# Kernel tuning notes

Hardware: AMD Instinct MI355X
Metric: run time of the kernel (lower is better)

## Reference

```python
import jax, jax.numpy as jnp
import numpy as np


def setup_inputs() -> dict:
    key = jax.random.key(0)
    k1, k2 = jax.random.split(key)
    B, K, S = 262144, 32, 30
    sparse_code = jax.random.normal(k1, (B, K), dtype=jnp.float32)
    dictionary = jax.random.normal(k2, (S * S, K), dtype=jnp.float32)
    return {"sparse_code": sparse_code, "dictionary": dictionary, "image_size": S}


def reference(sparse_code, dictionary, image_size):
    # matmul(dictionary, sparse_code.T).T == sparse_code @ dictionary.T -> [B, S*S]
    samples = jnp.einsum("bk,dk->bd", sparse_code, dictionary)
    B = samples.shape[0]
    img = samples.reshape(B, image_size, image_size)
    # Serpentine unrolling: flip every odd row (rows 1,3,...,image_size-1)
    img = img.at[:, 1::2, :].set(img[:, 1::2, ::-1])
    return img[:, None, :, :]  # [B, 1, S, S]
```

## Files before the change

kernel.cpp:

```cpp
#include <hip/hip_runtime.h>
#include <hip/hip_bf16.h>


typedef __attribute__((ext_vector_type(8))) short bf16x8;
typedef __attribute__((ext_vector_type(4))) float f32x4;

constexpr int KD    = 32;
constexpr int DDIM  = 900;
constexpr int SDIM  = 30;
constexpr int NCHT  = 57;
constexpr int TROWS = 16;
constexpr int TILES = 16;
constexpr int RPB   = TROWS * TILES;
constexpr int TFL   = TROWS * DDIM;

__device__ __forceinline__ int serp_src(int d) {
    int r = d / SDIM, c = d - r * SDIM;
    return (r & 1) ? (r * SDIM + (SDIM - 1 - c)) : d;
}

__device__ __forceinline__ short f2bf(float x) {
    __hip_bfloat16 h = __float2bfloat16(x);
    short u; __builtin_memcpy(&u, &h, 2); return u;
}

__device__ __forceinline__ void barrier_lds() {
    __builtin_amdgcn_sched_barrier(0);
    asm volatile("s_waitcnt lgkmcnt(0)" ::: "memory");
    __builtin_amdgcn_sched_barrier(0);
    __builtin_amdgcn_s_barrier();
    __builtin_amdgcn_sched_barrier(0);
}

__global__ __launch_bounds__(256, 1) void mfma_decode(
    const float* __restrict__ sc,
    const float* __restrict__ dict,
    float* __restrict__ out,
    int B)
{
    __shared__ alignas(16) float stg[2][TFL];

    const int t    = threadIdx.x;
    const int lane = t & 63;
    const int wid  = t >> 6;

    const int brow = lane & 15;
    const int k0   = (lane >> 4) << 3;
    const int dloc = (lane >> 4) << 2;
    const long long b0 = (long long)blockIdx.x * RPB;

    float4 ra[TILES], rb[TILES];
    #pragma unroll
    for (int tt = 0; tt < TILES; ++tt) {
        const float* ap = sc + (size_t)(b0 + tt * TROWS + brow) * KD + k0;
        ra[tt] = *reinterpret_cast<const float4*>(ap);
        rb[tt] = *reinterpret_cast<const float4*>(ap + 4);
    }

    bf16x8 df[15];
    #pragma unroll
    for (int j = 0; j < 15; ++j) {
        int ch = wid + 4 * j; if (ch > NCHT - 1) ch = NCHT - 1;
        int d  = ch * 16 + (lane & 15);
        int dd = (d < DDIM) ? d : (DDIM - 1);
        const float* p = dict + (size_t)serp_src(dd) * KD + k0;
        const float4 f0 = *reinterpret_cast<const float4*>(p);
        const float4 f1 = *reinterpret_cast<const float4*>(p + 4);
        bf16x8 a;
        a[0] = f2bf(f0.x); a[1] = f2bf(f0.y); a[2] = f2bf(f0.z); a[3] = f2bf(f0.w);
        a[4] = f2bf(f1.x); a[5] = f2bf(f1.y); a[6] = f2bf(f1.z); a[7] = f2bf(f1.w);
        df[j] = a;
    }

    bf16x8 bb[TILES];
    #pragma unroll
    for (int tt = 0; tt < TILES; ++tt) {
        bf16x8 r;
        r[0] = f2bf(ra[tt].x); r[1] = f2bf(ra[tt].y);
        r[2] = f2bf(ra[tt].z); r[3] = f2bf(ra[tt].w);
        r[4] = f2bf(rb[tt].x); r[5] = f2bf(rb[tt].y);
        r[6] = f2bf(rb[tt].z); r[7] = f2bf(rb[tt].w);
        bb[tt] = r;
    }

    auto compute = [&](const bf16x8& bbx, float* buf) {
        #pragma unroll
        for (int j = 0; j < 15; ++j) {
            const int ch = wid + 4 * j;
            if (ch < NCHT) {
                f32x4 z = {0.f, 0.f, 0.f, 0.f};
                f32x4 acc = __builtin_amdgcn_mfma_f32_16x16x32_bf16(df[j], bbx, z, 0, 0, 0);
                if (ch != 56) {
                    *reinterpret_cast<f32x4*>(&buf[brow * DDIM + ch * 16 + dloc]) = acc;
                } else if (dloc == 0) {
                    *reinterpret_cast<f32x4*>(&buf[brow * DDIM + 896]) = acc;
                }
            }
        }
    };

    compute(bb[0], stg[0]);
    barrier_lds();

    const int base = t * 4;

    #pragma unroll
    for (int tile = 0; tile < TILES; ++tile) {
        if (tile + 1 < TILES) compute(bb[tile + 1], stg[(tile + 1) & 1]);

        float* __restrict__ tbase = out + (size_t)(b0 + (long long)tile * TROWS) * DDIM;
        const float* __restrict__ buf = stg[tile & 1];
        #pragma unroll
        for (int i = 0; i < 14; ++i) {
            const int o = i * 1024 + base;
            f32x4 v = *reinterpret_cast<const f32x4*>(&buf[o]);
            *reinterpret_cast<f32x4*>(tbase + o) = v;
        }
        if (t < 16) {
            const int o = 14336 + base;
            f32x4 v = *reinterpret_cast<const f32x4*>(&buf[o]);
            *reinterpret_cast<f32x4*>(tbase + o) = v;
        }

        if (tile + 1 < TILES) barrier_lds();
    }
}

extern "C" void kernel_launch(void* const* d_in, const int* in_sizes, int n_in,
                              void* d_out, int out_size, void* d_ws, size_t ws_size,
                              hipStream_t stream) {
    const float* sc   = (const float*)d_in[0];
    const float* dict = (const float*)d_in[1];
    float* out        = (float*)d_out;

    const int B = in_sizes[0] / KD;

    mfma_decode<<<dim3((unsigned)(B / RPB)), 256, 0, stream>>>(sc, dict, out, B);
}
```

Baseline: 194.9 us.

## Specialize warps into MFMA producers and global-store consumers with 512 threads

The block doubles to 512 threads. Waves 0-3 load the dictionary and codes, run the MFMA tiles and write them into double-buffered LDS, while waves 4-7 only copy finished tiles from LDS to global memory. The aim is to overlap compute with the store-bound output traffic through producer/consumer specialization. The cost is an extra barrier per tile, and the store loop now has half the waves doing all the writes, which may reduce store parallelism per wave.

After: 195.1 us. About the same (+0.1%).

```diff
diff --git a/kernel.cpp b/kernel.cpp
--- a/kernel.cpp
+++ b/kernel.cpp
@@ -32,7 +32,7 @@
     __builtin_amdgcn_sched_barrier(0);
 }
 
-__global__ __launch_bounds__(256, 1) void mfma_decode(
+__global__ __launch_bounds__(512, 1) void mfma_decode(
     const float* __restrict__ sc,
     const float* __restrict__ dict,
     float* __restrict__ out,
@@ -49,39 +49,8 @@
     const int dloc = (lane >> 4) << 2;
     const long long b0 = (long long)blockIdx.x * RPB;
 
-    float4 ra[TILES], rb[TILES];
-    #pragma unroll
-    for (int tt = 0; tt < TILES; ++tt) {
-        const float* ap = sc + (size_t)(b0 + tt * TROWS + brow) * KD + k0;
-        ra[tt] = *reinterpret_cast<const float4*>(ap);
-        rb[tt] = *reinterpret_cast<const float4*>(ap + 4);
-    }
-
     bf16x8 df[15];
-    #pragma unroll
-    for (int j = 0; j < 15; ++j) {
-        int ch = wid + 4 * j; if (ch > NCHT - 1) ch = NCHT - 1;
-        int d  = ch * 16 + (lane & 15);
-        int dd = (d < DDIM) ? d : (DDIM - 1);
-        const float* p = dict + (size_t)serp_src(dd) * KD + k0;
-        const float4 f0 = *reinterpret_cast<const float4*>(p);
-        const float4 f1 = *reinterpret_cast<const float4*>(p + 4);
-        bf16x8 a;
-        a[0] = f2bf(f0.x); a[1] = f2bf(f0.y); a[2] = f2bf(f0.z); a[3] = f2bf(f0.w);
-        a[4] = f2bf(f1.x); a[5] = f2bf(f1.y); a[6] = f2bf(f1.z); a[7] = f2bf(f1.w);
-        df[j] = a;
-    }
-
     bf16x8 bb[TILES];
-    #pragma unroll
-    for (int tt = 0; tt < TILES; ++tt) {
-        bf16x8 r;
-        r[0] = f2bf(ra[tt].x); r[1] = f2bf(ra[tt].y);
-        r[2] = f2bf(ra[tt].z); r[3] = f2bf(ra[tt].w);
-        r[4] = f2bf(rb[tt].x); r[5] = f2bf(rb[tt].y);
-        r[6] = f2bf(rb[tt].z); r[7] = f2bf(rb[tt].w);
-        bb[tt] = r;
-    }
 
     auto compute = [&](const bf16x8& bbx, float* buf) {
         #pragma unroll
@@ -99,30 +68,69 @@
         }
     };
 
-    compute(bb[0], stg[0]);
+    if (wid < 4) {
+        #pragma unroll
+        for (int j = 0; j < 15; ++j) {
+            int ch = wid + 4 * j; if (ch > NCHT - 1) ch = NCHT - 1;
+            int d  = ch * 16 + (lane & 15);
+            int dd = (d < DDIM) ? d : (DDIM - 1);
+            const float* p = dict + (size_t)serp_src(dd) * KD + k0;
+            const float4 f0 = *reinterpret_cast<const float4*>(p);
+            const float4 f1 = *reinterpret_cast<const float4*>(p + 4);
+            bf16x8 a;
+            a[0] = f2bf(f0.x); a[1] = f2bf(f0.y); a[2] = f2bf(f0.z); a[3] = f2bf(f0.w);
+            a[4] = f2bf(f1.x); a[5] = f2bf(f1.y); a[6] = f2bf(f1.z); a[7] = f2bf(f1.w);
+            df[j] = a;
+        }
+
+        #pragma unroll
+        for (int g = 0; g < TILES / 4; ++g) {
+            float4 ra[4], rb[4];
+            #pragma unroll
+            for (int u = 0; u < 4; ++u) {
+                const int tt = g * 4 + u;
+                const float* ap = sc + (size_t)(b0 + tt * TROWS + brow) * KD + k0;
+                ra[u] = *reinterpret_cast<const float4*>(ap);
+                rb[u] = *reinterpret_cast<const float4*>(ap + 4);
+            }
+            #pragma unroll
+            for (int u = 0; u < 4; ++u) {
+                bf16x8 r;
+                r[0] = f2bf(ra[u].x); r[1] = f2bf(ra[u].y);
+                r[2] = f2bf(ra[u].z); r[3] = f2bf(ra[u].w);
+                r[4] = f2bf(rb[u].x); r[5] = f2bf(rb[u].y);
+                r[6] = f2bf(rb[u].z); r[7] = f2bf(rb[u].w);
+                bb[g * 4 + u] = r;
+            }
+        }
+
+        compute(bb[0], stg[0]);
+    }
     barrier_lds();
 
-    const int base = t * 4;
+    const int base = (t - 256) * 4;
 
     #pragma unroll
     for (int tile = 0; tile < TILES; ++tile) {
-        if (tile + 1 < TILES) compute(bb[tile + 1], stg[(tile + 1) & 1]);
-
-        float* __restrict__ tbase = out + (size_t)(b0 + (long long)tile * TROWS) * DDIM;
-        const float* __restrict__ buf = stg[tile & 1];
-        #pragma unroll
-        for (int i = 0; i < 14; ++i) {
-            const int o = i * 1024 + base;
-            f32x4 v = *reinterpret_cast<const f32x4*>(&buf[o]);
-            *reinterpret_cast<f32x4*>(tbase + o) = v;
+        if (wid < 4) {
+            if (tile + 1 < TILES) compute(bb[tile + 1], stg[(tile + 1) & 1]);
+        } else {
+            const float* __restrict__ buf = stg[tile & 1];
+            float* __restrict__ tbase =
+                out + (size_t)(b0 + (long long)tile * TROWS) * DDIM;
+            #pragma unroll
+            for (int i = 0; i < 14; ++i) {
+                const int o = i * 1024 + base;
+                f32x4 v = *reinterpret_cast<const f32x4*>(&buf[o]);
+                *reinterpret_cast<f32x4*>(tbase + o) = v;
+            }
+            if (t < 272) {
+                const int o = 14336 + base;
+                f32x4 v = *reinterpret_cast<const f32x4*>(&buf[o]);
+                *reinterpret_cast<f32x4*>(tbase + o) = v;
+            }
         }
-        if (t < 16) {
-            const int o = 14336 + base;
-            f32x4 v = *reinterpret_cast<const f32x4*>(&buf[o]);
-            *reinterpret_cast<f32x4*>(tbase + o) = v;
-        }
-
-        if (tile + 1 < TILES) barrier_lds();
+        barrier_lds();
     }
 }
 
@@ -135,5 +143,5 @@
 
     const int B = in_sizes[0] / KD;
 
-    mfma_decode<<<dim3((unsigned)(B / RPB)), 256, 0, stream>>>(sc, dict, out, B);
+    mfma_decode<<<dim3((unsigned)(B / RPB)), 512, 0, stream>>>(sc, dict, out, B);
 }
```
